# Optimization experiments

Hardware: AMD Instinct MI355X
Metric: run time of the kernel (lower is better)

## Reference

```python
import jax, jax.numpy as jnp
import numpy as np

N, E, C = 8192, 8192, 256
AVG_DEG = 32


def _linear(x, w, b):
    return x @ w + b


def setup_inputs() -> dict:
    key = jax.random.key(0)
    ks = jax.random.split(key, 20)
    s = 1.0 / np.sqrt(C)
    x = jax.random.normal(ks[0], (N, C), dtype=jnp.float32)
    # binary adjacency with avg degree ~32 (unweighted COO -> dense 0/1 rep)
    adj = (jax.random.uniform(ks[1], (N, N)) < (AVG_DEG / N)).astype(jnp.float32)
    tar_ei = jax.random.randint(ks[2], (2, E), 0, N, dtype=jnp.int32)
    p = {
        'xlin_w1': jax.random.uniform(ks[3], (C, C), minval=-s, maxval=s),
        'xlin_b1': jnp.zeros((C,), jnp.float32),
        'xlin_w2': jax.random.uniform(ks[4], (C, C), minval=-s, maxval=s),
        'xlin_b2': jnp.zeros((C,), jnp.float32),
        'xcn_w1': jax.random.uniform(ks[5], (C, C), minval=-s, maxval=s),
        'xcn_b1': jnp.zeros((C,), jnp.float32),
        'xcn_w2': jax.random.uniform(ks[6], (C, C), minval=-s, maxval=s),
        'xcn_b2': jnp.zeros((C,), jnp.float32),
        'xij_w': jax.random.uniform(ks[7], (C, C), minval=-s, maxval=s),
        'xij_b': jnp.zeros((C,), jnp.float32),
        'lin_w1': jax.random.uniform(ks[8], (C, C), minval=-s, maxval=s),
        'lin_b1': jnp.zeros((C,), jnp.float32),
        'lin_w2': jax.random.uniform(ks[9], (C, 1), minval=-s, maxval=s),
        'lin_b2': jnp.zeros((1,), jnp.float32),
        'beta': jnp.ones((1,), jnp.float32),
    }
    return {'x': x, 'adj': adj, 'tar_ei': tar_ei, **p}


def reference(x, adj, tar_ei,
              xlin_w1, xlin_b1, xlin_w2, xlin_b2,
              xcn_w1, xcn_b1, xcn_w2, xcn_b2,
              xij_w, xij_b,
              lin_w1, lin_b1, lin_w2, lin_b2, beta):
    i, j = tar_ei[0], tar_ei[1]
    xi = x[i]                      # [E, C]
    xj = x[j]                      # [E, C]
    # x = x + xlin(x): Linear-ReLU-Linear-ReLU (dropout inactive, ln=Identity)
    h = x + jax.nn.relu(_linear(jax.nn.relu(_linear(x, xlin_w1, xlin_b1)), xlin_w2, xlin_b2))
    # adjoverlap: common-neighbor mask per target edge, cn[e,k] = A[i_e,k]*A[j_e,k]
    cn = adj[i] * adj[j]           # [E, N]
    # spmm_add(cn, h)
    xcn = cn @ h                   # [E, C]
    # xijlin: Linear-ReLU (tailact -> Identity tail)
    xij = jax.nn.relu(_linear(xi * xj, xij_w, xij_b))
    # xcnlin: Linear-ReLU-Linear-ReLU
    xcn = jax.nn.relu(_linear(jax.nn.relu(_linear(xcn, xcn_w1, xcn_b1)), xcn_w2, xcn_b2))
    # lin: Linear-ReLU-Linear(out)
    z = xcn * beta + xij
    out = _linear(jax.nn.relu(_linear(z, lin_w1, lin_b1)), lin_w2, lin_b2)
    return out  # [E, 1]
```

## Files before the change

kernel.cpp:

```cpp
#include <hip/hip_runtime.h>
#include <cstdint>
#include <cstddef>


#define C_DIM   256
#define N_NODES 8192
#define E_EDGES 8192

typedef short bf16x8 __attribute__((ext_vector_type(8)));
typedef float f32x4  __attribute__((ext_vector_type(4)));

struct WPtrs { const float* p[6]; };

__device__ __forceinline__ unsigned short bf16_rne(float a) {
    unsigned u = __float_as_uint(a);
    u += 0x7FFFu + ((u >> 16) & 1u);
    return (unsigned short)(u >> 16);
}
__device__ __forceinline__ void split2(float v, short& h, short& l) {
    unsigned short hb = bf16_rne(v);
    h = (short)hb;
    l = (short)bf16_rne(v - __uint_as_float((unsigned)hb << 16));
}
__device__ __forceinline__ float bf2f(short h) {
    return __uint_as_float(((unsigned)(unsigned short)h) << 16);
}

__global__ __launch_bounds__(256) void k_prep(const float* __restrict__ adj,
                                              unsigned long long* __restrict__ bits,
                                              WPtrs wp, short* __restrict__ WFH,
                                              short* __restrict__ WFL) {
    const int t = threadIdx.x;
    if (blockIdx.x < 48) {
        __shared__ float tile[32][257];
        const int g  = blockIdx.x >> 3;
        const int kf = blockIdx.x & 7;
        const float* W = wp.p[g];
        #pragma unroll
        for (int p = 0; p < 8; ++p) {
            int s = t + (p << 8);
            int row = s >> 6, c4 = s & 63;
            float4 v = *(const float4*)&W[(size_t)(kf * 32 + row) * C_DIM + (c4 << 2)];
            tile[row][(c4 << 2) + 0] = v.x; tile[row][(c4 << 2) + 1] = v.y;
            tile[row][(c4 << 2) + 2] = v.z; tile[row][(c4 << 2) + 3] = v.w;
        }
        __syncthreads();
        #pragma unroll
        for (int p = 0; p < 4; ++p) {
            int s = t + (p << 8);
            int nf = s >> 6, lane = s & 63;
            int q = lane >> 4, fr = lane & 15;
            short h[8], l[8];
            #pragma unroll
            for (int e = 0; e < 8; ++e)
                split2(tile[q * 8 + e][nf * 16 + fr], h[e], l[e]);
            int dst = (g << 16) + (((kf * 16 + nf) << 6) + lane) * 8;
            *(short4*)&WFH[dst]     = make_short4(h[0], h[1], h[2], h[3]);
            *(short4*)&WFH[dst + 4] = make_short4(h[4], h[5], h[6], h[7]);
            *(short4*)&WFL[dst]     = make_short4(l[0], l[1], l[2], l[3]);
            *(short4*)&WFL[dst + 4] = make_short4(l[4], l[5], l[6], l[7]);
        }
    } else {
        const int TOTALW = N_NODES * N_NODES / 64;
        const int gw   = ((int)blockIdx.x - 48) * 4 + (t >> 6);
        const int lane = t & 63;
        const int NW   = 2048 * 4;
        for (int w = gw << 3; w < TOTALW; w += NW << 3) {
            float v[8];
            #pragma unroll
            for (int r = 0; r < 8; ++r)
                v[r] = adj[((size_t)(w + r) << 6) + lane];
            unsigned long long m[8];
            #pragma unroll
            for (int r = 0; r < 8; ++r)
                m[r] = __ballot(v[r] > 0.5f);
            if (lane == 0) {
                #pragma unroll
                for (int r = 0; r < 4; ++r) {
                    ulonglong2 u2; u2.x = m[2 * r]; u2.y = m[2 * r + 1];
                    *(ulonglong2*)&bits[w + 2 * r] = u2;
                }
            }
        }
    }
}

__device__ __forceinline__ void layer_core(
    const short (*INH)[C_DIM], const short (*INL)[C_DIM],
    const short* __restrict__ WH, f32x4 acc[2])
{
    const int t = threadIdx.x, lane = t & 63, wq = t >> 6;
    const int fr = lane & 15, q = lane >> 4;
    #pragma unroll
    for (int i = 0; i < 2; ++i)
        #pragma unroll
        for (int r = 0; r < 4; ++r) acc[i][r] = 0.f;
    #pragma unroll 2
    for (int kf = 0; kf < 8; ++kf) {
        bf16x8 aH[2], aL[2];
        #pragma unroll
        for (int mf = 0; mf < 2; ++mf) {
            const int row = mf * 16 + fr;
            const int cc = (((kf << 2) + q) ^ (row & 7)) << 3;
            aH[mf] = *(const bf16x8*)&INH[row][cc];
            aL[mf] = *(const bf16x8*)&INL[row][cc];
        }
        const int wo = (((kf << 4) + wq) * 64 + lane) * 8;
        bf16x8 bH = *(const bf16x8*)&WH[wo];
        #pragma unroll
        for (int mf = 0; mf < 2; ++mf) {
            acc[mf] = __builtin_amdgcn_mfma_f32_16x16x32_bf16(aH[mf], bH, acc[mf], 0, 0, 0);
            acc[mf] = __builtin_amdgcn_mfma_f32_16x16x32_bf16(aL[mf], bH, acc[mf], 0, 0, 0);
        }
    }
}

__global__ __launch_bounds__(1024, 1) void k_edge_mega(
    const unsigned long long* __restrict__ bits, const float* __restrict__ x,
    const int* __restrict__ tar,
    const short* __restrict__ WFH,
    const float* __restrict__ b1x, const float* __restrict__ b2x,
    const float* __restrict__ bxij, const float* __restrict__ bcn1,
    const float* __restrict__ bcn2, const float* __restrict__ blin1,
    const float* __restrict__ betap, const float* __restrict__ w2,
    const float* __restrict__ b2o, float* __restrict__ out)
{
    __shared__ short AH[32][C_DIM], AL[32][C_DIM];
    __shared__ short BH[32][C_DIM], BL[32][C_DIM];
    __shared__ int   eij2[32][2];
    __shared__ int   inst[1024];
    __shared__ int   cntot;
    __shared__ float out32[32];
    const int e0 = blockIdx.x << 5;
    const int t = threadIdx.x;
    const int lane = t & 63, wq = t >> 6;
    const int fr = lane & 15, q = lane >> 4;
    const int et = t >> 5;
    const int c8 = (t & 31) << 3;

    if (t < 32) {
        eij2[t][0] = tar[e0 + t];
        eij2[t][1] = tar[E_EDGES + e0 + t];
        out32[t] = 0.f;
    }
    if (t == 0) cntot = 0;
    __syncthreads();

    #pragma unroll
    for (int p = 0; p < 8; ++p) {
        int idx = (p << 10) + t;
        int e = idx >> 8, c = idx & 255;
        float v = x[(size_t)eij2[e][0] * C_DIM + c] * x[(size_t)eij2[e][1] * C_DIM + c];
        short h, l;
        split2(v, h, l);
        int cw = (((c >> 3) ^ (e & 7)) << 3) + (c & 7);
        BH[e][cw] = h;
        BL[e][cw] = l;
    }
    {
        const int le = t >> 5, sub = t & 31;
        const size_t bi = (size_t)eij2[le][0] * 128;
        const size_t bj = (size_t)eij2[le][1] * 128;
        #pragma unroll
        for (int w4 = 0; w4 < 4; ++w4) {
            const int w = (sub << 2) + w4;
            unsigned long long m = bits[bi + w] & bits[bj + w];
            while (m) {
                int b = __builtin_ctzll(m);
                int slot = atomicAdd(&cntot, 1);
                if (slot < 1024) inst[slot] = (le << 16) | ((w << 6) + b);
                m &= m - 1;
            }
        }
    }
    __syncthreads();

    float xijr[2][4];
    {
        f32x4 acc[2];
        layer_core(BH, BL, WFH + 2 * 65536, acc);
        const int col = (wq << 4) + fr;
        const float bb = bxij[col];
        #pragma unroll
        for (int mf = 0; mf < 2; ++mf)
            #pragma unroll
            for (int r = 0; r < 4; ++r)
                xijr[mf][r] = fmaxf(acc[mf][r] + bb, 0.f);
    }

    float xcnreg[8];
    #pragma unroll
    for (int u = 0; u < 8; ++u) xcnreg[u] = 0.f;
    const int ctot = min(cntot, 1024);
    for (int c0 = 0; c0 < ctot; c0 += 32) {
        const int nrows = min(32, ctot - c0);
        #pragma unroll
        for (int p = 0; p < 8; ++p) {
            int idx = (p << 10) + t;
            int r = idx >> 8, c = idx & 255;
            float v = 0.f;
            if (r < nrows) {
                int k = inst[c0 + r] & 0xffff;
                v = x[(size_t)k * C_DIM + c];
            }
            short h, l;
            split2(v, h, l);
            int cw = (((c >> 3) ^ (r & 7)) << 3) + (c & 7);
            AH[r][cw] = h;
            AL[r][cw] = l;
        }
        __syncthreads();
        {
            f32x4 acc[2];
            layer_core(AH, AL, WFH + 0 * 65536, acc);
            const int col = (wq << 4) + fr;
            const float bb = b1x[col];
            #pragma unroll
            for (int mf = 0; mf < 2; ++mf)
                #pragma unroll
                for (int r = 0; r < 4; ++r) {
                    const int row = mf * 16 + q * 4 + r;
                    float v = fmaxf(acc[mf][r] + bb, 0.f);
                    short h, l;
                    split2(v, h, l);
                    const int cw = (((col >> 3) ^ (row & 7)) << 3) + (col & 7);
                    BH[row][cw] = h;
                    BL[row][cw] = l;
                }
        }
        __syncthreads();
        {
            f32x4 acc[2];
            layer_core(BH, BL, WFH + 1 * 65536, acc);
            const int col = (wq << 4) + fr;
            const float bb = b2x[col];
            #pragma unroll
            for (int mf = 0; mf < 2; ++mf)
                #pragma unroll
                for (int r = 0; r < 4; ++r) {
                    const int row = mf * 16 + q * 4 + r;
                    if (row < nrows) {
                        const int k = inst[c0 + row] & 0xffff;
                        float v = fmaxf(acc[mf][r] + bb, 0.f) +
                                  x[(size_t)k * C_DIM + col];
                        short h, l;
                        split2(v, h, l);
                        const int cw = (((col >> 3) ^ (row & 7)) << 3) + (col & 7);
                        AH[row][cw] = h;
                        AL[row][cw] = l;
                    }
                }
        }
        __syncthreads();
        for (int s = 0; s < nrows; ++s) {
            int pk = inst[c0 + s];
            if ((pk >> 16) == et) {
                const int cw = ((c8 >> 3) ^ (s & 7)) << 3;
                short4 h0 = *(const short4*)&AH[s][cw];
                short4 h1 = *(const short4*)&AH[s][cw + 4];
                short4 l0 = *(const short4*)&AL[s][cw];
                short4 l1 = *(const short4*)&AL[s][cw + 4];
                xcnreg[0] += bf2f(h0.x) + bf2f(l0.x);
                xcnreg[1] += bf2f(h0.y) + bf2f(l0.y);
                xcnreg[2] += bf2f(h0.z) + bf2f(l0.z);
                xcnreg[3] += bf2f(h0.w) + bf2f(l0.w);
                xcnreg[4] += bf2f(h1.x) + bf2f(l1.x);
                xcnreg[5] += bf2f(h1.y) + bf2f(l1.y);
                xcnreg[6] += bf2f(h1.z) + bf2f(l1.z);
                xcnreg[7] += bf2f(h1.w) + bf2f(l1.w);
            }
        }
        __syncthreads();
    }

    {
        const int cwb = ((c8 >> 3) ^ (et & 7)) << 3;
        short h[8], l[8];
        #pragma unroll
        for (int u = 0; u < 8; ++u) split2(xcnreg[u], h[u], l[u]);
        *(short4*)&AH[et][cwb]     = make_short4(h[0], h[1], h[2], h[3]);
        *(short4*)&AH[et][cwb + 4] = make_short4(h[4], h[5], h[6], h[7]);
        *(short4*)&AL[et][cwb]     = make_short4(l[0], l[1], l[2], l[3]);
        *(short4*)&AL[et][cwb + 4] = make_short4(l[4], l[5], l[6], l[7]);
    }
    __syncthreads();

    const float beta = betap[0];
    {
        f32x4 acc[2];
        layer_core(AH, AL, WFH + 3 * 65536, acc);
        const int col = (wq << 4) + fr;
        const float bb = bcn1[col];
        #pragma unroll
        for (int mf = 0; mf < 2; ++mf)
            #pragma unroll
            for (int r = 0; r < 4; ++r) {
                const int row = mf * 16 + q * 4 + r;
                float v = fmaxf(acc[mf][r] + bb, 0.f);
                short h, l;
                split2(v, h, l);
                const int cw = (((col >> 3) ^ (row & 7)) << 3) + (col & 7);
                BH[row][cw] = h;
                BL[row][cw] = l;
            }
    }
    __syncthreads();
    {
        f32x4 acc[2];
        layer_core(BH, BL, WFH + 4 * 65536, acc);
        const int col = (wq << 4) + fr;
        const float bb = bcn2[col];
        #pragma unroll
        for (int mf = 0; mf < 2; ++mf)
            #pragma unroll
            for (int r = 0; r < 4; ++r) {
                const int row = mf * 16 + q * 4 + r;
                float v = fmaxf(acc[mf][r] + bb, 0.f) * beta + xijr[mf][r];
                short h, l;
                split2(v, h, l);
                const int cw = (((col >> 3) ^ (row & 7)) << 3) + (col & 7);
                AH[row][cw] = h;
                AL[row][cw] = l;
            }
    }
    __syncthreads();
    {
        f32x4 acc[2];
        layer_core(AH, AL, WFH + 5 * 65536, acc);
        const int col = (wq << 4) + fr;
        const float bb = blin1[col];
        const float w2c = w2[col];
        #pragma unroll
        for (int mf = 0; mf < 2; ++mf) {
            #pragma unroll
            for (int r = 0; r < 4; ++r) {
                float s = fmaxf(acc[mf][r] + bb, 0.f) * w2c;
                s += __shfl_xor(s, 1); s += __shfl_xor(s, 2);
                s += __shfl_xor(s, 4); s += __shfl_xor(s, 8);
                if (fr == 0) atomicAdd(&out32[mf * 16 + q * 4 + r], s);
            }
        }
    }
    __syncthreads();
    if (t < 32) out[e0 + t] = out32[t] + b2o[0];
}

extern "C" void kernel_launch(void* const* d_in, const int* in_sizes, int n_in,
                              void* d_out, int out_size, void* d_ws, size_t ws_size,
                              hipStream_t stream) {
    const float* x       = (const float*)d_in[0];
    const float* adj     = (const float*)d_in[1];
    const int*   tar_ei  = (const int*)  d_in[2];
    const float* xlin_w1 = (const float*)d_in[3];
    const float* xlin_b1 = (const float*)d_in[4];
    const float* xlin_w2 = (const float*)d_in[5];
    const float* xlin_b2 = (const float*)d_in[6];
    const float* xcn_w1  = (const float*)d_in[7];
    const float* xcn_b1  = (const float*)d_in[8];
    const float* xcn_w2  = (const float*)d_in[9];
    const float* xcn_b2  = (const float*)d_in[10];
    const float* xij_w   = (const float*)d_in[11];
    const float* xij_b   = (const float*)d_in[12];
    const float* lin_w1  = (const float*)d_in[13];
    const float* lin_b1  = (const float*)d_in[14];
    const float* lin_w2  = (const float*)d_in[15];
    const float* lin_b2  = (const float*)d_in[16];
    const float* beta    = (const float*)d_in[17];
    float* out = (float*)d_out;

    char* ws = (char*)d_ws;
    const size_t MB = 1024 * 1024;
    unsigned long long* bits = (unsigned long long*)(ws);
    short* WFH  = (short*)(ws +  8 * MB);
    short* WFL  = (short*)(ws +  9 * MB);

    WPtrs wp;
    wp.p[0] = xlin_w1; wp.p[1] = xlin_w2; wp.p[2] = xij_w;
    wp.p[3] = xcn_w1;  wp.p[4] = xcn_w2;  wp.p[5] = lin_w1;

    hipLaunchKernelGGL(k_prep, dim3(48 + 2048), dim3(256), 0, stream,
                       adj, bits, wp, WFH, WFL);
    hipLaunchKernelGGL(k_edge_mega, dim3(E_EDGES / 32), dim3(1024), 0, stream,
                       bits, x, tar_ei, WFH,
                       xlin_b1, xlin_b2, xij_b, xcn_b1, xcn_b2, lin_b1,
                       beta, lin_w2, lin_b2, out);
}
```

Measured before the change: 79.16 us.

## Merge prep and edge kernels into one persistent kernel with global counters

Folds the weight-split and adjacency-bitpacking prep into the edge kernel. All 256 blocks pack their slice of the adjacency, and the first 48 also convert weights, then they synchronise through global atomic counters. The xij layer now runs before waiting for the bitmask, overlapping it with other blocks finishing the packing, and the unused low-weight writes are dropped. This removes one kernel launch boundary but adds a memset and spin-waits that rely on all 256 blocks being co-resident.

```diff
diff --git a/kernel.cpp b/kernel.cpp
--- a/kernel.cpp
+++ b/kernel.cpp
@@ -22,50 +22,119 @@
     h = (short)hb;
     l = (short)bf16_rne(v - __uint_as_float((unsigned)hb << 16));
 }
-__device__ __forceinline__ float bf2f(short h) {
-    return __uint_as_float(((unsigned)(unsigned short)h) << 16);
-}
-
-__global__ __launch_bounds__(256) void k_prep(const float* __restrict__ adj,
-                                              unsigned long long* __restrict__ bits,
-                                              WPtrs wp, short* __restrict__ WFH,
-                                              short* __restrict__ WFL) {
+
+__device__ __forceinline__ void block_signal(unsigned* c) {
+    __syncthreads();
+    if (threadIdx.x == 0) {
+        __threadfence();
+        __hip_atomic_fetch_add(c, 1u, __ATOMIC_RELEASE, __HIP_MEMORY_SCOPE_AGENT);
+    }
+}
+__device__ __forceinline__ void block_wait(const unsigned* c, unsigned tgt) {
+    if (threadIdx.x == 0) {
+        while (__hip_atomic_load(c, __ATOMIC_ACQUIRE, __HIP_MEMORY_SCOPE_AGENT) < tgt)
+            __builtin_amdgcn_s_sleep(32);
+    }
+    __syncthreads();
+    __threadfence();
+}
+
+__device__ __forceinline__ void layer_core(
+    const short (*INH)[C_DIM], const short (*INL)[C_DIM],
+    const short* __restrict__ WH, f32x4 acc[2])
+{
+    const int t = threadIdx.x, lane = t & 63, wq = t >> 6;
+    const int fr = lane & 15, q = lane >> 4;
+    #pragma unroll
+    for (int i = 0; i < 2; ++i)
+        #pragma unroll
+        for (int r = 0; r < 4; ++r) acc[i][r] = 0.f;
+    #pragma unroll 2
+    for (int kf = 0; kf < 8; ++kf) {
+        bf16x8 aH[2], aL[2];
+        #pragma unroll
+        for (int mf = 0; mf < 2; ++mf) {
+            const int row = mf * 16 + fr;
+            const int cc = (((kf << 2) + q) ^ (row & 7)) << 3;
+            aH[mf] = *(const bf16x8*)&INH[row][cc];
+            aL[mf] = *(const bf16x8*)&INL[row][cc];
+        }
+        const int wo = (((kf << 4) + wq) * 64 + lane) * 8;
+        bf16x8 bH = *(const bf16x8*)&WH[wo];
+        #pragma unroll
+        for (int mf = 0; mf < 2; ++mf) {
+            acc[mf] = __builtin_amdgcn_mfma_f32_16x16x32_bf16(aH[mf], bH, acc[mf], 0, 0, 0);
+            acc[mf] = __builtin_amdgcn_mfma_f32_16x16x32_bf16(aL[mf], bH, acc[mf], 0, 0, 0);
+        }
+    }
+}
+
+__global__ __launch_bounds__(1024, 1) void k_all(
+    const float* __restrict__ adj, const float* __restrict__ x,
+    const int* __restrict__ tar, WPtrs wp,
+    unsigned long long* __restrict__ bits, short* __restrict__ WFH,
+    unsigned* __restrict__ ctrs,
+    const float* __restrict__ b1x, const float* __restrict__ b2x,
+    const float* __restrict__ bxij, const float* __restrict__ bcn1,
+    const float* __restrict__ bcn2, const float* __restrict__ blin1,
+    const float* __restrict__ betap, const float* __restrict__ w2,
+    const float* __restrict__ b2o, float* __restrict__ out)
+{
+    __shared__ float wtile[32][257];
+    __shared__ short AH[32][C_DIM], AL[32][C_DIM];
+    __shared__ short BH[32][C_DIM], BL[32][C_DIM];
+    __shared__ int   eij2[32][2];
+    __shared__ int   inst[1024];
+    __shared__ int   cntot;
+    __shared__ float out32[32];
+    const int bid = blockIdx.x;
     const int t = threadIdx.x;
-    if (blockIdx.x < 48) {
-        __shared__ float tile[32][257];
-        const int g  = blockIdx.x >> 3;
-        const int kf = blockIdx.x & 7;
+    const int lane = t & 63, wq = t >> 6;
+    const int fr = lane & 15, q = lane >> 4;
+    const int et = t >> 5;
+    const int c8 = (t & 31) << 3;
+    unsigned* wctr = ctrs;
+    unsigned* bctr = ctrs + 1;
+
+    if (t < 32) {
+        eij2[t][0] = tar[(bid << 5) + t];
+        eij2[t][1] = tar[E_EDGES + (bid << 5) + t];
+        out32[t] = 0.f;
+    }
+    if (t == 0) cntot = 0;
+
+    if (bid < 48) {
+        const int g  = bid >> 3;
+        const int kf = bid & 7;
         const float* W = wp.p[g];
         #pragma unroll
-        for (int p = 0; p < 8; ++p) {
-            int s = t + (p << 8);
+        for (int p = 0; p < 2; ++p) {
+            int s = t + (p << 10);
             int row = s >> 6, c4 = s & 63;
             float4 v = *(const float4*)&W[(size_t)(kf * 32 + row) * C_DIM + (c4 << 2)];
-            tile[row][(c4 << 2) + 0] = v.x; tile[row][(c4 << 2) + 1] = v.y;
-            tile[row][(c4 << 2) + 2] = v.z; tile[row][(c4 << 2) + 3] = v.w;
+            wtile[row][(c4 << 2) + 0] = v.x; wtile[row][(c4 << 2) + 1] = v.y;
+            wtile[row][(c4 << 2) + 2] = v.z; wtile[row][(c4 << 2) + 3] = v.w;
         }
         __syncthreads();
-        #pragma unroll
-        for (int p = 0; p < 4; ++p) {
-            int s = t + (p << 8);
-            int nf = s >> 6, lane = s & 63;
-            int q = lane >> 4, fr = lane & 15;
-            short h[8], l[8];
+        {
+            int nf = t >> 6, ln = t & 63;
+            int qq = ln >> 4, ff = ln & 15;
+            short h[8], lx;
             #pragma unroll
             for (int e = 0; e < 8; ++e)
-                split2(tile[q * 8 + e][nf * 16 + fr], h[e], l[e]);
-            int dst = (g << 16) + (((kf * 16 + nf) << 6) + lane) * 8;
+                split2(wtile[qq * 8 + e][nf * 16 + ff], h[e], lx);
+            int dst = (g << 16) + (((kf * 16 + nf) << 6) + ln) * 8;
             *(short4*)&WFH[dst]     = make_short4(h[0], h[1], h[2], h[3]);
             *(short4*)&WFH[dst + 4] = make_short4(h[4], h[5], h[6], h[7]);
-            *(short4*)&WFL[dst]     = make_short4(l[0], l[1], l[2], l[3]);
-            *(short4*)&WFL[dst + 4] = make_short4(l[4], l[5], l[6], l[7]);
-        }
-    } else {
-        const int TOTALW = N_NODES * N_NODES / 64;
-        const int gw   = ((int)blockIdx.x - 48) * 4 + (t >> 6);
-        const int lane = t & 63;
-        const int NW   = 2048 * 4;
-        for (int w = gw << 3; w < TOTALW; w += NW << 3) {
+        }
+        block_signal(wctr);
+    }
+
+    {
+        const int gw = (bid << 4) + wq;
+        const int w0 = gw << 8;
+        for (int it = 0; it < 32; ++it) {
+            const int w = w0 + (it << 3);
             float v[8];
             #pragma unroll
             for (int r = 0; r < 8; ++r)
@@ -82,69 +151,8 @@
                 }
             }
         }
-    }
-}
-
-__device__ __forceinline__ void layer_core(
-    const short (*INH)[C_DIM], const short (*INL)[C_DIM],
-    const short* __restrict__ WH, f32x4 acc[2])
-{
-    const int t = threadIdx.x, lane = t & 63, wq = t >> 6;
-    const int fr = lane & 15, q = lane >> 4;
-    #pragma unroll
-    for (int i = 0; i < 2; ++i)
-        #pragma unroll
-        for (int r = 0; r < 4; ++r) acc[i][r] = 0.f;
-    #pragma unroll 2
-    for (int kf = 0; kf < 8; ++kf) {
-        bf16x8 aH[2], aL[2];
-        #pragma unroll
-        for (int mf = 0; mf < 2; ++mf) {
-            const int row = mf * 16 + fr;
-            const int cc = (((kf << 2) + q) ^ (row & 7)) << 3;
-            aH[mf] = *(const bf16x8*)&INH[row][cc];
-            aL[mf] = *(const bf16x8*)&INL[row][cc];
-        }
-        const int wo = (((kf << 4) + wq) * 64 + lane) * 8;
-        bf16x8 bH = *(const bf16x8*)&WH[wo];
-        #pragma unroll
-        for (int mf = 0; mf < 2; ++mf) {
-            acc[mf] = __builtin_amdgcn_mfma_f32_16x16x32_bf16(aH[mf], bH, acc[mf], 0, 0, 0);
-            acc[mf] = __builtin_amdgcn_mfma_f32_16x16x32_bf16(aL[mf], bH, acc[mf], 0, 0, 0);
-        }
-    }
-}
-
-__global__ __launch_bounds__(1024, 1) void k_edge_mega(
-    const unsigned long long* __restrict__ bits, const float* __restrict__ x,
-    const int* __restrict__ tar,
-    const short* __restrict__ WFH,
-    const float* __restrict__ b1x, const float* __restrict__ b2x,
-    const float* __restrict__ bxij, const float* __restrict__ bcn1,
-    const float* __restrict__ bcn2, const float* __restrict__ blin1,
-    const float* __restrict__ betap, const float* __restrict__ w2,
-    const float* __restrict__ b2o, float* __restrict__ out)
-{
-    __shared__ short AH[32][C_DIM], AL[32][C_DIM];
-    __shared__ short BH[32][C_DIM], BL[32][C_DIM];
-    __shared__ int   eij2[32][2];
-    __shared__ int   inst[1024];
-    __shared__ int   cntot;
-    __shared__ float out32[32];
-    const int e0 = blockIdx.x << 5;
-    const int t = threadIdx.x;
-    const int lane = t & 63, wq = t >> 6;
-    const int fr = lane & 15, q = lane >> 4;
-    const int et = t >> 5;
-    const int c8 = (t & 31) << 3;
-
-    if (t < 32) {
-        eij2[t][0] = tar[e0 + t];
-        eij2[t][1] = tar[E_EDGES + e0 + t];
-        out32[t] = 0.f;
-    }
-    if (t == 0) cntot = 0;
-    __syncthreads();
+        block_signal(bctr);
+    }
 
     #pragma unroll
     for (int p = 0; p < 8; ++p) {
@@ -157,6 +165,23 @@
         BH[e][cw] = h;
         BL[e][cw] = l;
     }
+    __syncthreads();
+
+    block_wait(wctr, 48);
+    float xijr[2][4];
+    {
+        f32x4 acc[2];
+        layer_core(BH, BL, WFH + 2 * 65536, acc);
+        const int col = (wq << 4) + fr;
+        const float bb = bxij[col];
+        #pragma unroll
+        for (int mf = 0; mf < 2; ++mf)
+            #pragma unroll
+            for (int r = 0; r < 4; ++r)
+                xijr[mf][r] = fmaxf(acc[mf][r] + bb, 0.f);
+    }
+
+    block_wait(bctr, 256);
     {
         const int le = t >> 5, sub = t & 31;
         const size_t bi = (size_t)eij2[le][0] * 128;
@@ -174,19 +199,6 @@
         }
     }
     __syncthreads();
-
-    float xijr[2][4];
-    {
-        f32x4 acc[2];
-        layer_core(BH, BL, WFH + 2 * 65536, acc);
-        const int col = (wq << 4) + fr;
-        const float bb = bxij[col];
-        #pragma unroll
-        for (int mf = 0; mf < 2; ++mf)
-            #pragma unroll
-            for (int r = 0; r < 4; ++r)
-                xijr[mf][r] = fmaxf(acc[mf][r] + bb, 0.f);
-    }
 
     float xcnreg[8];
     #pragma unroll
@@ -260,14 +272,16 @@
                 short4 h1 = *(const short4*)&AH[s][cw + 4];
                 short4 l0 = *(const short4*)&AL[s][cw];
                 short4 l1 = *(const short4*)&AL[s][cw + 4];
-                xcnreg[0] += bf2f(h0.x) + bf2f(l0.x);
-                xcnreg[1] += bf2f(h0.y) + bf2f(l0.y);
-                xcnreg[2] += bf2f(h0.z) + bf2f(l0.z);
-                xcnreg[3] += bf2f(h0.w) + bf2f(l0.w);
-                xcnreg[4] += bf2f(h1.x) + bf2f(l1.x);
-                xcnreg[5] += bf2f(h1.y) + bf2f(l1.y);
-                xcnreg[6] += bf2f(h1.z) + bf2f(l1.z);
-                xcnreg[7] += bf2f(h1.w) + bf2f(l1.w);
+                #define BF(hh) __uint_as_float(((unsigned)(unsigned short)(hh)) << 16)
+                xcnreg[0] += BF(h0.x) + BF(l0.x);
+                xcnreg[1] += BF(h0.y) + BF(l0.y);
+                xcnreg[2] += BF(h0.z) + BF(l0.z);
+                xcnreg[3] += BF(h0.w) + BF(l0.w);
+                xcnreg[4] += BF(h1.x) + BF(l1.x);
+                xcnreg[5] += BF(h1.y) + BF(l1.y);
+                xcnreg[6] += BF(h1.z) + BF(l1.z);
+                xcnreg[7] += BF(h1.w) + BF(l1.w);
+                #undef BF
             }
         }
         __syncthreads();
@@ -342,7 +356,7 @@
         }
     }
     __syncthreads();
-    if (t < 32) out[e0 + t] = out32[t] + b2o[0];
+    if (t < 32) out[(bid << 5) + t] = out32[t] + b2o[0];
 }
 
 extern "C" void kernel_launch(void* const* d_in, const int* in_sizes, int n_in,
@@ -371,17 +385,16 @@
     char* ws = (char*)d_ws;
     const size_t MB = 1024 * 1024;
     unsigned long long* bits = (unsigned long long*)(ws);
-    short* WFH  = (short*)(ws +  8 * MB);
-    short* WFL  = (short*)(ws +  9 * MB);
+    short*    WFH  = (short*)(ws + 8 * MB);
+    unsigned* ctrs = (unsigned*)(ws + 9 * MB);
 
     WPtrs wp;
     wp.p[0] = xlin_w1; wp.p[1] = xlin_w2; wp.p[2] = xij_w;
     wp.p[3] = xcn_w1;  wp.p[4] = xcn_w2;  wp.p[5] = lin_w1;
 
-    hipLaunchKernelGGL(k_prep, dim3(48 + 2048), dim3(256), 0, stream,
-                       adj, bits, wp, WFH, WFL);
-    hipLaunchKernelGGL(k_edge_mega, dim3(E_EDGES / 32), dim3(1024), 0, stream,
-                       bits, x, tar_ei, WFH,
+    hipMemsetAsync(ctrs, 0, 2 * sizeof(unsigned), stream);
+    hipLaunchKernelGGL(k_all, dim3(256), dim3(1024), 0, stream,
+                       adj, x, tar_ei, wp, bits, WFH, ctrs,
                        xlin_b1, xlin_b2, xij_b, xcn_b1, xcn_b2, lin_b1,
                        beta, lin_w2, lin_b2, out);
 }
```

After: 242.7 us. +206.6%, slower.

## Halve edges per block and remap MFMA tiles to two N-fragments per wave

Applied to the files above, without the earlier changes.

Each block now handles 16 target edges with 512 threads instead of 32 edges with 1024 threads, so the grid doubles to 512 blocks. The launch bound changes from (1024,1) to (512,8). In the shared MLP core, each wave now computes one 16-row M fragment across two 16-column N fragments, instead of two M fragments across one N fragment. The goal is to put more, smaller blocks on the CUs so latency is better hidden and tails are shorter. The cost is that each wave loads twice as many weight fragments, so total weight traffic from L2 per edge doubles.

```diff
diff --git a/kernel.cpp b/kernel.cpp
--- a/kernel.cpp
+++ b/kernel.cpp
@@ -97,25 +97,21 @@
         for (int r = 0; r < 4; ++r) acc[i][r] = 0.f;
     #pragma unroll 2
     for (int kf = 0; kf < 8; ++kf) {
-        bf16x8 aH[2], aL[2];
-        #pragma unroll
-        for (int mf = 0; mf < 2; ++mf) {
-            const int row = mf * 16 + fr;
-            const int cc = (((kf << 2) + q) ^ (row & 7)) << 3;
-            aH[mf] = *(const bf16x8*)&INH[row][cc];
-            aL[mf] = *(const bf16x8*)&INL[row][cc];
-        }
-        const int wo = (((kf << 4) + wq) * 64 + lane) * 8;
-        bf16x8 bH = *(const bf16x8*)&WH[wo];
-        #pragma unroll
-        for (int mf = 0; mf < 2; ++mf) {
-            acc[mf] = __builtin_amdgcn_mfma_f32_16x16x32_bf16(aH[mf], bH, acc[mf], 0, 0, 0);
-            acc[mf] = __builtin_amdgcn_mfma_f32_16x16x32_bf16(aL[mf], bH, acc[mf], 0, 0, 0);
-        }
-    }
-}
-
-__global__ __launch_bounds__(1024, 1) void k_edge_mega(
+        const int cc = (((kf << 2) + q) ^ (fr & 7)) << 3;
+        bf16x8 aH = *(const bf16x8*)&INH[fr][cc];
+        bf16x8 aL = *(const bf16x8*)&INL[fr][cc];
+        #pragma unroll
+        for (int nl = 0; nl < 2; ++nl) {
+            const int nf = (wq << 1) + nl;
+            const int wo = (((kf << 4) + nf) * 64 + lane) * 8;
+            bf16x8 bH = *(const bf16x8*)&WH[wo];
+            acc[nl] = __builtin_amdgcn_mfma_f32_16x16x32_bf16(aH, bH, acc[nl], 0, 0, 0);
+            acc[nl] = __builtin_amdgcn_mfma_f32_16x16x32_bf16(aL, bH, acc[nl], 0, 0, 0);
+        }
+    }
+}
+
+__global__ __launch_bounds__(512, 8) void k_edge(
     const unsigned long long* __restrict__ bits, const float* __restrict__ x,
     const int* __restrict__ tar,
     const short* __restrict__ WFH,
@@ -125,30 +121,30 @@
     const float* __restrict__ betap, const float* __restrict__ w2,
     const float* __restrict__ b2o, float* __restrict__ out)
 {
-    __shared__ short AH[32][C_DIM], AL[32][C_DIM];
-    __shared__ short BH[32][C_DIM], BL[32][C_DIM];
-    __shared__ int   eij2[32][2];
-    __shared__ int   inst[1024];
+    __shared__ short AH[16][C_DIM], AL[16][C_DIM];
+    __shared__ short BH[16][C_DIM], BL[16][C_DIM];
+    __shared__ int   eij2[16][2];
+    __shared__ int   inst[512];
     __shared__ int   cntot;
-    __shared__ float out32[32];
-    const int e0 = blockIdx.x << 5;
+    __shared__ float out16[16];
+    const int e0 = blockIdx.x << 4;
     const int t = threadIdx.x;
     const int lane = t & 63, wq = t >> 6;
     const int fr = lane & 15, q = lane >> 4;
     const int et = t >> 5;
     const int c8 = (t & 31) << 3;
 
-    if (t < 32) {
+    if (t < 16) {
         eij2[t][0] = tar[e0 + t];
         eij2[t][1] = tar[E_EDGES + e0 + t];
-        out32[t] = 0.f;
+        out16[t] = 0.f;
     }
     if (t == 0) cntot = 0;
     __syncthreads();
 
     #pragma unroll
     for (int p = 0; p < 8; ++p) {
-        int idx = (p << 10) + t;
+        int idx = (p << 9) + t;
         int e = idx >> 8, c = idx & 255;
         float v = x[(size_t)eij2[e][0] * C_DIM + c] * x[(size_t)eij2[e][1] * C_DIM + c];
         short h, l;
@@ -168,7 +164,7 @@
             while (m) {
                 int b = __builtin_ctzll(m);
                 int slot = atomicAdd(&cntot, 1);
-                if (slot < 1024) inst[slot] = (le << 16) | ((w << 6) + b);
+                if (slot < 512) inst[slot] = (le << 16) | ((w << 6) + b);
                 m &= m - 1;
             }
         }
@@ -179,24 +175,25 @@
     {
         f32x4 acc[2];
         layer_core(BH, BL, WFH + 2 * 65536, acc);
-        const int col = (wq << 4) + fr;
-        const float bb = bxij[col];
-        #pragma unroll
-        for (int mf = 0; mf < 2; ++mf)
+        #pragma unroll
+        for (int nl = 0; nl < 2; ++nl) {
+            const int col = ((wq << 1) + nl) * 16 + fr;
+            const float bb = bxij[col];
             #pragma unroll
             for (int r = 0; r < 4; ++r)
-                xijr[mf][r] = fmaxf(acc[mf][r] + bb, 0.f);
+                xijr[nl][r] = fmaxf(acc[nl][r] + bb, 0.f);
+        }
     }
 
     float xcnreg[8];
     #pragma unroll
     for (int u = 0; u < 8; ++u) xcnreg[u] = 0.f;
-    const int ctot = min(cntot, 1024);
-    for (int c0 = 0; c0 < ctot; c0 += 32) {
-        const int nrows = min(32, ctot - c0);
+    const int ctot = min(cntot, 512);
+    for (int c0 = 0; c0 < ctot; c0 += 16) {
+        const int nrows = min(16, ctot - c0);
         #pragma unroll
         for (int p = 0; p < 8; ++p) {
-            int idx = (p << 10) + t;
+            int idx = (p << 9) + t;
             int r = idx >> 8, c = idx & 255;
             float v = 0.f;
             if (r < nrows) {
@@ -213,35 +210,36 @@
         {
             f32x4 acc[2];
             layer_core(AH, AL, WFH + 0 * 65536, acc);
-            const int col = (wq << 4) + fr;
-            const float bb = b1x[col];
-            #pragma unroll
-            for (int mf = 0; mf < 2; ++mf)
+            #pragma unroll
+            for (int nl = 0; nl < 2; ++nl) {
+                const int col = ((wq << 1) + nl) * 16 + fr;
+                const float bb = b1x[col];
                 #pragma unroll
                 for (int r = 0; r < 4; ++r) {
-                    const int row = mf * 16 + q * 4 + r;
-                    float v = fmaxf(acc[mf][r] + bb, 0.f);
+                    const int row = q * 4 + r;
+                    float v = fmaxf(acc[nl][r] + bb, 0.f);
                     short h, l;
                     split2(v, h, l);
                     const int cw = (((col >> 3) ^ (row & 7)) << 3) + (col & 7);
                     BH[row][cw] = h;
                     BL[row][cw] = l;
                 }
+            }
         }
         __syncthreads();
         {
             f32x4 acc[2];
             layer_core(BH, BL, WFH + 1 * 65536, acc);
-            const int col = (wq << 4) + fr;
-            const float bb = b2x[col];
-            #pragma unroll
-            for (int mf = 0; mf < 2; ++mf)
+            #pragma unroll
+            for (int nl = 0; nl < 2; ++nl) {
+                const int col = ((wq << 1) + nl) * 16 + fr;
+                const float bb = b2x[col];
                 #pragma unroll
                 for (int r = 0; r < 4; ++r) {
-                    const int row = mf * 16 + q * 4 + r;
+                    const int row = q * 4 + r;
                     if (row < nrows) {
                         const int k = inst[c0 + row] & 0xffff;
-                        float v = fmaxf(acc[mf][r] + bb, 0.f) +
+                        float v = fmaxf(acc[nl][r] + bb, 0.f) +
                                   x[(size_t)k * C_DIM + col];
                         short h, l;
                         split2(v, h, l);
@@ -250,6 +248,7 @@
                         AL[row][cw] = l;
                     }
                 }
+            }
         }
         __syncthreads();
         for (int s = 0; s < nrows; ++s) {
@@ -289,60 +288,62 @@
     {
         f32x4 acc[2];
         layer_core(AH, AL, WFH + 3 * 65536, acc);
-        const int col = (wq << 4) + fr;
-        const float bb = bcn1[col];
-        #pragma unroll
-        for (int mf = 0; mf < 2; ++mf)
+        #pragma unroll
+        for (int nl = 0; nl < 2; ++nl) {
+            const int col = ((wq << 1) + nl) * 16 + fr;
+            const float bb = bcn1[col];
             #pragma unroll
             for (int r = 0; r < 4; ++r) {
-                const int row = mf * 16 + q * 4 + r;
-                float v = fmaxf(acc[mf][r] + bb, 0.f);
+                const int row = q * 4 + r;
+                float v = fmaxf(acc[nl][r] + bb, 0.f);
                 short h, l;
                 split2(v, h, l);
                 const int cw = (((col >> 3) ^ (row & 7)) << 3) + (col & 7);
                 BH[row][cw] = h;
                 BL[row][cw] = l;
             }
+        }
     }
     __syncthreads();
     {
         f32x4 acc[2];
         layer_core(BH, BL, WFH + 4 * 65536, acc);
-        const int col = (wq << 4) + fr;
-        const float bb = bcn2[col];
-        #pragma unroll
-        for (int mf = 0; mf < 2; ++mf)
+        #pragma unroll
+        for (int nl = 0; nl < 2; ++nl) {
+            const int col = ((wq << 1) + nl) * 16 + fr;
+            const float bb = bcn2[col];
             #pragma unroll
             for (int r = 0; r < 4; ++r) {
-                const int row = mf * 16 + q * 4 + r;
-                float v = fmaxf(acc[mf][r] + bb, 0.f) * beta + xijr[mf][r];
+                const int row = q * 4 + r;
+                float v = fmaxf(acc[nl][r] + bb, 0.f) * beta + xijr[nl][r];
                 short h, l;
                 split2(v, h, l);
                 const int cw = (((col >> 3) ^ (row & 7)) << 3) + (col & 7);
                 AH[row][cw] = h;
                 AL[row][cw] = l;
             }
+        }
     }
     __syncthreads();
     {
         f32x4 acc[2];
         layer_core(AH, AL, WFH + 5 * 65536, acc);
-        const int col = (wq << 4) + fr;
-        const float bb = blin1[col];
-        const float w2c = w2[col];
-        #pragma unroll
-        for (int mf = 0; mf < 2; ++mf) {
+        #pragma unroll
+        for (int nl = 0; nl < 2; ++nl) {
+            const int col = ((wq << 1) + nl) * 16 + fr;
+            const float bb = blin1[col];
+            const float w2c = w2[col];
             #pragma unroll
             for (int r = 0; r < 4; ++r) {
-                float s = fmaxf(acc[mf][r] + bb, 0.f) * w2c;
+                float s = fmaxf(acc[nl][r] + bb, 0.f) * w2c;
                 s += __shfl_xor(s, 1); s += __shfl_xor(s, 2);
                 s += __shfl_xor(s, 4); s += __shfl_xor(s, 8);
-                if (fr == 0) atomicAdd(&out32[mf * 16 + q * 4 + r], s);
-            }
-        }
-    }
-    __syncthreads();
-    if (t < 32) out[e0 + t] = out32[t] + b2o[0];
+                if (fr == 0) atomicAdd(&out16[q * 4 + r], s);
+            }
+        }
+    }
+    __syncthreads();
+    if (t < 16) out[e0 + t] = out16[t] + b2o[0];
 }
 
 extern "C" void kernel_launch(void* const* d_in, const int* in_sizes, int n_in,
@@ -380,7 +381,7 @@
 
     hipLaunchKernelGGL(k_prep, dim3(48 + 2048), dim3(256), 0, stream,
                        adj, bits, wp, WFH, WFL);
-    hipLaunchKernelGGL(k_edge_mega, dim3(E_EDGES / 32), dim3(1024), 0, stream,
+    hipLaunchKernelGGL(k_edge, dim3(E_EDGES / 16), dim3(512), 0, stream,
                        bits, x, tar_ei, WFH,
                        xlin_b1, xlin_b2, xij_b, xcn_b1, xcn_b2, lin_b1,
                        beta, lin_w2, lin_b2, out);
```

Result: slower. 127.8 us (+61.5%).
